# Kernel tuning notes

Hardware: AMD Instinct MI355X
Metric: run time of the kernel (lower is better)

Reference implementation:

```python
import jax, jax.numpy as jnp
import numpy as np

B, S, D, H, W, FFN = 2, 4096, 1024, 16, 256, 4096
HD = D // H


def layer_norm(x, g, b):
    mu = x.mean(-1, keepdims=True)
    var = ((x - mu) ** 2).mean(-1, keepdims=True)
    return (x - mu) * jax.lax.rsqrt(var + 1e-5) * g + b


def setup_inputs() -> dict:
    key = jax.random.key(0)
    ks = jax.random.split(key, 16)
    s = 1.0 / np.sqrt(D)
    inp = {
        "x": jax.random.normal(ks[0], (B, S, D), jnp.float32),
        "Wq": jax.random.normal(ks[1], (D, D), jnp.float32) * s,
        "bq": jnp.zeros((D,), jnp.float32),
        "Wk": jax.random.normal(ks[2], (D, D), jnp.float32) * s,
        "bk": jnp.zeros((D,), jnp.float32),
        "Wv": jax.random.normal(ks[3], (D, D), jnp.float32) * s,
        "bv": jnp.zeros((D,), jnp.float32),
        "Wo": jax.random.normal(ks[4], (D, D), jnp.float32) * s,
        "bo": jnp.zeros((D,), jnp.float32),
        "g1": jnp.ones((D,), jnp.float32),
        "b1": jnp.zeros((D,), jnp.float32),
        "W1": jax.random.normal(ks[5], (D, FFN), jnp.float32) * s,
        "c1": jnp.zeros((FFN,), jnp.float32),
        "W2": jax.random.normal(ks[6], (FFN, D), jnp.float32) * (1.0 / np.sqrt(FFN)),
        "c2": jnp.zeros((D,), jnp.float32),
        "g2": jnp.ones((D,), jnp.float32),
        "b2": jnp.zeros((D,), jnp.float32),
    }
    return inp


def sliding_window_attn(x, Wq, bq, Wk, bk, Wv, bv, Wo, bo):
    b, s, d = x.shape
    nb = s // W
    # project and chunk into blocks of size W: (B, nb, W, H, HD)
    q = (x @ Wq + bq).reshape(b, nb, W, H, HD)
    k = (x @ Wk + bk).reshape(b, nb, W, H, HD)
    v = (x @ Wv + bv).reshape(b, nb, W, H, HD)
    pad = [(0, 0), (1, 1), (0, 0), (0, 0), (0, 0)]
    kp, vp = jnp.pad(k, pad), jnp.pad(v, pad)
    # each block attends to [prev, self, next] blocks -> (B, nb, 3W, H, HD)
    kc = jnp.concatenate([kp[:, :-2], kp[:, 1:-1], kp[:, 2:]], axis=2)
    vc = jnp.concatenate([vp[:, :-2], vp[:, 1:-1], vp[:, 2:]], axis=2)
    scale = jnp.asarray(1.0 / np.sqrt(HD), x.dtype)
    scores = jnp.einsum("bnqhd,bnkhd->bhnqk", q, kc) * scale
    i = jnp.arange(W)[:, None]
    j = jnp.arange(3 * W)[None, :]
    band = jnp.abs(i + W - j) <= W  # (W, 3W): |q_pos - k_pos| <= W
    kidx = jnp.arange(nb)[:, None] * W - W + jnp.arange(3 * W)[None, :]
    valid = (kidx >= 0) & (kidx < s)  # (nb, 3W): drop padded halo blocks
    mask = band[None, :, :] & valid[:, None, :]  # (nb, W, 3W)
    scores = jnp.where(mask[None, None], scores, jnp.asarray(-1e9, x.dtype))
    attn = jax.nn.softmax(scores, axis=-1)
    out = jnp.einsum("bhnqk,bnkhd->bnqhd", attn, vc).reshape(b, s, d)
    return out @ Wo + bo


def reference(x, Wq, bq, Wk, bk, Wv, bv, Wo, bo, g1, b1, W1, c1, W2, c2, g2, b2):
    a = sliding_window_attn(x, Wq, bq, Wk, bk, Wv, bv, Wo, bo)
    h = layer_norm(a + x, g1, b1)  # dropout = identity (eval mode)
    f = jax.nn.gelu(h @ W1 + c1) @ W2 + c2
    return layer_norm(f + h, g2, b2)
```

## Files before the change

kernel.cpp:

```cpp
#include <hip/hip_runtime.h>
#include <hip/hip_bf16.h>

#define BB 2
#define SS 4096
#define DD 1024
#define HH 16
#define WW 256
#define FF 4096
#define HDIM 64
#define NBLK (SS / WW)
#define MROWS (BB * SS)

typedef short bfrag8 __attribute__((ext_vector_type(8)));
typedef float floatx4 __attribute__((ext_vector_type(4)));

__device__ __forceinline__ float bf2f(ushort u) {
    union { uint i; float f; } c; c.i = ((uint)u) << 16; return c.f;
}
__device__ __forceinline__ ushort f2bf(float f) {
    union { float f; uint i; } c; c.f = f;
    uint r = (c.i + 0x7FFFu + ((c.i >> 16) & 1u)) >> 16;
    return (ushort)r;
}
__device__ __forceinline__ float gelu_fast(float x) {
    float z2 = 1.5957691216057308f * x * (1.f + 0.044715f * x * x);
    return x / (1.f + __expf(-z2));
}

__device__ __forceinline__ void gload_lds16(const ushort* g, ushort* l) {
    __builtin_amdgcn_global_load_lds(
        (const __attribute__((address_space(1))) void*)g,
        (__attribute__((address_space(3))) void*)l, 16, 0, 0);
}

__global__ __launch_bounds__(256) void cvt_f32_bf16(
    const float* __restrict__ in, ushort* __restrict__ out)
{
    size_t i = ((size_t)blockIdx.x * 256 + threadIdx.x) * 4;
    float4 v = *(const float4*)(in + i);
    union { ushort u[4]; uint2 d; } t;
    t.u[0] = f2bf(v.x); t.u[1] = f2bf(v.y);
    t.u[2] = f2bf(v.z); t.u[3] = f2bf(v.w);
    *(uint2*)(out + i) = t.d;
}

__global__ __launch_bounds__(256) void cvt_transpose_all(
    const float* __restrict__ Wq, const float* __restrict__ Wk,
    const float* __restrict__ Wv, const float* __restrict__ Wo,
    const float* __restrict__ W1, const float* __restrict__ W2,
    ushort* __restrict__ WqkvT, ushort* __restrict__ WoT,
    ushort* __restrict__ W1t, ushort* __restrict__ W2t)
{
    __shared__ ushort sT[32][33];
    const int z = blockIdx.z;
    const float* in; ushort* out; int K, N, n0, k0;
    if (z < 4) {
        if (blockIdx.x >= 32) return;
        in  = (z == 0) ? Wq : (z == 1) ? Wk : (z == 2) ? Wv : Wo;
        out = (z < 3) ? WqkvT + (size_t)z * 1024 * 1024 : WoT;
        K = 1024; N = 1024;
        n0 = blockIdx.x * 32; k0 = blockIdx.y * 32;
    } else if (z == 4) {
        in = W1; out = W1t; K = 1024; N = 4096;
        n0 = blockIdx.x * 32; k0 = blockIdx.y * 32;
    } else {
        in = W2; out = W2t; K = 4096; N = 1024;
        n0 = blockIdx.y * 32; k0 = blockIdx.x * 32;
    }

    const int r  = threadIdx.x >> 3;
    const int c4 = (threadIdx.x & 7) * 4;

    float4 v = *(const float4*)(in + (size_t)(k0 + r) * N + n0 + c4);
    sT[c4 + 0][r] = f2bf(v.x);
    sT[c4 + 1][r] = f2bf(v.y);
    sT[c4 + 2][r] = f2bf(v.z);
    sT[c4 + 3][r] = f2bf(v.w);
    __syncthreads();
    union { ushort u[4]; uint2 d; } t;
#pragma unroll
    for (int e = 0; e < 4; ++e) t.u[e] = sT[r][c4 + e];
    *(uint2*)(out + (size_t)(n0 + r) * K + k0 + c4) = t.d;
}

__global__ __launch_bounds__(256) void gemm_bt(
    const ushort* __restrict__ A, const ushort* __restrict__ Bt,
    const float* __restrict__ bias, ushort* __restrict__ C,
    int M, int N, int K, int act)
{
    __shared__ ushort sA[128 * 32];
    __shared__ ushort sB[128 * 32];

    const int tid  = threadIdx.x;
    const int m0   = blockIdx.y * 128;
    const int n0   = blockIdx.x * 128;
    const int wave = tid >> 6;
    const int lane = tid & 63;
    const int wm   = (wave >> 1) * 64;
    const int wn   = (wave & 1) * 64;
    const int lrow = lane & 15;
    const int quad = lane >> 4;

    floatx4 acc[4][4];
#pragma unroll
    for (int i = 0; i < 4; ++i)
#pragma unroll
        for (int j = 0; j < 4; ++j)
            acc[i][j] = (floatx4){0.f, 0.f, 0.f, 0.f};

    for (int k0 = 0; k0 < K; k0 += 32) {
#pragma unroll
        for (int it = 0; it < 2; ++it) {
            int c = it * 256 + tid;
            gload_lds16(A  + (size_t)(m0 + (c >> 2)) * K + k0 + (c & 3) * 8, &sA[c * 8]);
            gload_lds16(Bt + (size_t)(n0 + (c >> 2)) * K + k0 + (c & 3) * 8, &sB[c * 8]);
        }
        __syncthreads();

        bfrag8 af[4], bfv[4];
#pragma unroll
        for (int mt = 0; mt < 4; ++mt)
            af[mt] = *(const bfrag8*)&sA[(wm + mt * 16 + lrow) * 32 + quad * 8];
#pragma unroll
        for (int nt = 0; nt < 4; ++nt)
            bfv[nt] = *(const bfrag8*)&sB[(wn + nt * 16 + lrow) * 32 + quad * 8];
#pragma unroll
        for (int mt = 0; mt < 4; ++mt)
#pragma unroll
            for (int nt = 0; nt < 4; ++nt)
                acc[mt][nt] = __builtin_amdgcn_mfma_f32_16x16x32_bf16(
                    bfv[nt], af[mt], acc[mt][nt], 0, 0, 0);
        __syncthreads();
    }

#pragma unroll
    for (int nt = 0; nt < 4; ++nt) {
        int nb = n0 + wn + nt * 16 + quad * 4;
        union { float4 v; float f[4]; } b4;
        b4.v = *(const float4*)(bias + nb);
#pragma unroll
        for (int mt = 0; mt < 4; ++mt) {
            int row = m0 + wm + mt * 16 + lrow;
            union { ushort u[4]; uint2 d; } t;
#pragma unroll
            for (int r = 0; r < 4; ++r) {
                float v = acc[mt][nt][r] + b4.f[r];
                if (act) v = gelu_fast(v);
                t.u[r] = f2bf(v);
            }
            *(uint2*)(C + (size_t)row * N + nb) = t.d;
        }
    }
}

__global__ __launch_bounds__(256) void gemm_qkv(
    const ushort* __restrict__ A, const ushort* __restrict__ Bt,
    const float* __restrict__ bq, const float* __restrict__ bk,
    const float* __restrict__ bv,
    ushort* __restrict__ qb, ushort* __restrict__ kb, ushort* __restrict__ vT)
{
    __shared__ ushort sA[128 * 32];
    __shared__ ushort sB[128 * 32];
    const int K = DD;

    const int tid  = threadIdx.x;
    const int m0   = blockIdx.y * 128;
    const int n0   = blockIdx.x * 128;
    const int wave = tid >> 6;
    const int lane = tid & 63;
    const int wm   = (wave >> 1) * 64;
    const int wn   = (wave & 1) * 64;
    const int lrow = lane & 15;
    const int quad = lane >> 4;
    const int sel  = n0 >> 10;

    floatx4 acc[4][4];
#pragma unroll
    for (int i = 0; i < 4; ++i)
#pragma unroll
        for (int j = 0; j < 4; ++j)
            acc[i][j] = (floatx4){0.f, 0.f, 0.f, 0.f};

    if (sel < 2) {
        for (int k0 = 0; k0 < K; k0 += 32) {
#pragma unroll
            for (int it = 0; it < 2; ++it) {
                int c = it * 256 + tid;
                gload_lds16(A  + (size_t)(m0 + (c >> 2)) * K + k0 + (c & 3) * 8, &sA[c * 8]);
                gload_lds16(Bt + (size_t)(n0 + (c >> 2)) * K + k0 + (c & 3) * 8, &sB[c * 8]);
            }
            __syncthreads();
            bfrag8 af[4], bfv[4];
#pragma unroll
            for (int mt = 0; mt < 4; ++mt)
                af[mt] = *(const bfrag8*)&sA[(wm + mt * 16 + lrow) * 32 + quad * 8];
#pragma unroll
            for (int nt = 0; nt < 4; ++nt)
                bfv[nt] = *(const bfrag8*)&sB[(wn + nt * 16 + lrow) * 32 + quad * 8];
#pragma unroll
            for (int mt = 0; mt < 4; ++mt)
#pragma unroll
                for (int nt = 0; nt < 4; ++nt)
                    acc[mt][nt] = __builtin_amdgcn_mfma_f32_16x16x32_bf16(
                        bfv[nt], af[mt], acc[mt][nt], 0, 0, 0);
            __syncthreads();
        }
        ushort* C = (sel == 0) ? qb : kb;
        const float* bias = (sel == 0) ? bq : bk;
        const int colbase = n0 + wn;
#pragma unroll
        for (int nt = 0; nt < 4; ++nt) {
            int nb = (colbase + nt * 16 + quad * 4) & 1023;
            union { float4 v; float f[4]; } b4;
            b4.v = *(const float4*)(bias + nb);
#pragma unroll
            for (int mt = 0; mt < 4; ++mt) {
                int row = m0 + wm + mt * 16 + lrow;
                union { ushort u[4]; uint2 d; } t;
#pragma unroll
                for (int r = 0; r < 4; ++r) t.u[r] = f2bf(acc[mt][nt][r] + b4.f[r]);
                *(uint2*)(C + (size_t)row * DD + nb) = t.d;
            }
        }
    } else {
        for (int k0 = 0; k0 < K; k0 += 32) {
#pragma unroll
            for (int it = 0; it < 2; ++it) {
                int c = it * 256 + tid;
                gload_lds16(A  + (size_t)(m0 + (c >> 2)) * K + k0 + (c & 3) * 8, &sA[c * 8]);
                gload_lds16(Bt + (size_t)(n0 + (c >> 2)) * K + k0 + (c & 3) * 8, &sB[c * 8]);
            }
            __syncthreads();
            bfrag8 af[4], bfv[4];
#pragma unroll
            for (int mt = 0; mt < 4; ++mt)
                af[mt] = *(const bfrag8*)&sA[(wm + mt * 16 + lrow) * 32 + quad * 8];
#pragma unroll
            for (int nt = 0; nt < 4; ++nt)
                bfv[nt] = *(const bfrag8*)&sB[(wn + nt * 16 + lrow) * 32 + quad * 8];
#pragma unroll
            for (int mt = 0; mt < 4; ++mt)
#pragma unroll
                for (int nt = 0; nt < 4; ++nt)
                    acc[mt][nt] = __builtin_amdgcn_mfma_f32_16x16x32_bf16(
                        af[mt], bfv[nt], acc[mt][nt], 0, 0, 0);
            __syncthreads();
        }
        const int colbase = n0 + wn;
#pragma unroll
        for (int nt = 0; nt < 4; ++nt) {
            int cc = (colbase + nt * 16 + lrow) & 1023;
            int h = cc >> 6, dh = cc & 63;
            float bb = bv[cc];
#pragma unroll
            for (int mt = 0; mt < 4; ++mt) {
                int row0 = m0 + wm + mt * 16 + (quad << 2);
                int b = row0 >> 12, s = row0 & 4095;
                union { ushort u[4]; uint2 d; } t;
#pragma unroll
                for (int r = 0; r < 4; ++r) t.u[r] = f2bf(acc[mt][nt][r] + bb);
                *(uint2*)(vT + (size_t)(((b * HH + h) * HDIM + dh)) * SS + s) = t.d;
            }
        }
    }
}

__global__ __launch_bounds__(64, 2) void attn_flash(
    const ushort* __restrict__ q, const ushort* __restrict__ k,
    const ushort* __restrict__ vT, ushort* __restrict__ out)
{
    __shared__ ushort sP[64 * 72];

    const int qt = blockIdx.x, h = blockIdx.y, b = blockIdx.z;
    const int lane = threadIdx.x;
    const int c16  = lane & 15;
    const int quad = lane >> 4;
    const float CC = 0.18033688011112042f;

    bfrag8 qf[4][2];
    {
        const size_t qbase = ((size_t)b * SS + qt * 64) * DD + h * HDIM;
#pragma unroll
        for (int nt = 0; nt < 4; ++nt)
#pragma unroll
            for (int ks = 0; ks < 2; ++ks)
                qf[nt][ks] = *(const bfrag8*)(q + qbase +
                    (size_t)(nt * 16 + c16) * DD + ks * 32 + quad * 8);
    }

    floatx4 oacc[4][4];
#pragma unroll
    for (int i = 0; i < 4; ++i)
#pragma unroll
        for (int j = 0; j < 4; ++j)
            oacc[i][j] = (floatx4){0.f, 0.f, 0.f, 0.f};
    float mrow[4], lsum[4];
#pragma unroll
    for (int i = 0; i < 4; ++i) { mrow[i] = -1e30f; lsum[i] = 0.f; }

    const int st0 = (qt - 4 > 0) ? qt - 4 : 0;
    const int st1 = (qt + 4 < 63) ? qt + 4 : 63;
    const size_t kb_b  = (size_t)b * SS * DD + h * HDIM;
    const size_t vT_b  = (size_t)((b * HH + h) * HDIM) * SS;

    for (int st = st0; st <= st1; ++st) {
        const int dlt = st - qt;

        floatx4 sacc[4][4];
#pragma unroll
        for (int i = 0; i < 4; ++i)
#pragma unroll
            for (int j = 0; j < 4; ++j)
                sacc[i][j] = (floatx4){0.f, 0.f, 0.f, 0.f};
#pragma unroll
        for (int ks = 0; ks < 2; ++ks) {
            bfrag8 kf[4];
#pragma unroll
            for (int mt = 0; mt < 4; ++mt)
                kf[mt] = *(const bfrag8*)(k + kb_b +
                    (size_t)(st * 64 + mt * 16 + c16) * DD + ks * 32 + quad * 8);
#pragma unroll
            for (int mt = 0; mt < 4; ++mt)
#pragma unroll
                for (int nt = 0; nt < 4; ++nt)
                    sacc[mt][nt] = __builtin_amdgcn_mfma_f32_16x16x32_bf16(
                        kf[mt], qf[nt][ks], sacc[mt][nt], 0, 0, 0);
        }

        if (dlt == 4 || dlt == -4) {
#pragma unroll
            for (int mt = 0; mt < 4; ++mt)
#pragma unroll
                for (int nt = 0; nt < 4; ++nt)
#pragma unroll
                    for (int r = 0; r < 4; ++r) {
                        int kl = mt * 16 + quad * 4 + r;
                        int ql = nt * 16 + c16;
                        bool ok = (dlt < 0) ? (kl >= ql) : (kl <= ql);
                        if (!ok) sacc[mt][nt][r] = -1e30f;
                    }
        }

        float pm[4];
#pragma unroll
        for (int nt = 0; nt < 4; ++nt) {
            float a0 = fmaxf(fmaxf(sacc[0][nt][0], sacc[0][nt][1]),
                             fmaxf(sacc[0][nt][2], sacc[0][nt][3]));
            float a1 = fmaxf(fmaxf(sacc[1][nt][0], sacc[1][nt][1]),
                             fmaxf(sacc[1][nt][2], sacc[1][nt][3]));
            float a2 = fmaxf(fmaxf(sacc[2][nt][0], sacc[2][nt][1]),
                             fmaxf(sacc[2][nt][2], sacc[2][nt][3]));
            float a3 = fmaxf(fmaxf(sacc[3][nt][0], sacc[3][nt][1]),
                             fmaxf(sacc[3][nt][2], sacc[3][nt][3]));
            pm[nt] = fmaxf(fmaxf(a0, a1), fmaxf(a2, a3));
            pm[nt] = fmaxf(pm[nt], __shfl_xor(pm[nt], 16, 64));
            pm[nt] = fmaxf(pm[nt], __shfl_xor(pm[nt], 32, 64));
        }
        float al[4];
#pragma unroll
        for (int nt = 0; nt < 4; ++nt) {
            float mn = fmaxf(mrow[nt], pm[nt]);
            al[nt] = exp2f((mrow[nt] - mn) * CC);
            mrow[nt] = mn;
        }
        float ps[4] = {0.f, 0.f, 0.f, 0.f};
#pragma unroll
        for (int mt = 0; mt < 4; ++mt)
#pragma unroll
            for (int nt = 0; nt < 4; ++nt)
#pragma unroll
                for (int r = 0; r < 4; ++r) {
                    float p = exp2f((sacc[mt][nt][r] - mrow[nt]) * CC);
                    sacc[mt][nt][r] = p;
                    ps[nt] += p;
                }
#pragma unroll
        for (int nt = 0; nt < 4; ++nt) {
            ps[nt] += __shfl_xor(ps[nt], 16, 64);
            ps[nt] += __shfl_xor(ps[nt], 32, 64);
            lsum[nt] = lsum[nt] * al[nt] + ps[nt];
        }

#pragma unroll
        for (int mt = 0; mt < 4; ++mt)
#pragma unroll
            for (int nt = 0; nt < 4; ++nt) {
                int row = nt * 16 + c16;
                int g   = (2 * mt + (quad >> 1)) ^ (row & 3);
                union { ushort u[4]; uint2 d; } t;
#pragma unroll
                for (int r = 0; r < 4; ++r) t.u[r] = f2bf(sacc[mt][nt][r]);
                *(uint2*)&sP[row * 72 + g * 8 + (quad & 1) * 4] = t.d;
            }

#pragma unroll
        for (int dt = 0; dt < 4; ++dt)
#pragma unroll
            for (int nq = 0; nq < 4; ++nq)
#pragma unroll
                for (int r = 0; r < 4; ++r)
                    oacc[dt][nq][r] *= al[nq];

#pragma unroll
        for (int ks = 0; ks < 2; ++ks) {
            bfrag8 vf[4], pf[4];
#pragma unroll
            for (int dt = 0; dt < 4; ++dt)
                vf[dt] = *(const bfrag8*)(vT + vT_b +
                    (size_t)(dt * 16 + c16) * SS + st * 64 + ks * 32 + quad * 8);
#pragma unroll
            for (int nq = 0; nq < 4; ++nq) {
                int row = nq * 16 + c16;
                int g   = (4 * ks + quad) ^ (row & 3);
                pf[nq] = *(const bfrag8*)&sP[row * 72 + g * 8];
            }
#pragma unroll
            for (int dt = 0; dt < 4; ++dt)
#pragma unroll
                for (int nq = 0; nq < 4; ++nq)
                    oacc[dt][nq] = __builtin_amdgcn_mfma_f32_16x16x32_bf16(
                        vf[dt], pf[nq], oacc[dt][nq], 0, 0, 0);
        }
    }

#pragma unroll
    for (int nq = 0; nq < 4; ++nq) {
        float inv = 1.f / lsum[nq];
        size_t rbase = ((size_t)b * SS + qt * 64 + nq * 16 + c16) * DD + h * HDIM;
#pragma unroll
        for (int dt = 0; dt < 4; ++dt) {
            union { ushort u[4]; uint2 d; } t;
#pragma unroll
            for (int r = 0; r < 4; ++r) t.u[r] = f2bf(oacc[dt][nq][r] * inv);
            *(uint2*)(out + rbase + dt * 16 + quad * 4) = t.d;
        }
    }
}

__device__ __forceinline__ float ldv(const float* p)  { return *p; }
__device__ __forceinline__ float ldv(const ushort* p) { return bf2f(*p); }
__device__ __forceinline__ void  stv(float* p, float v)  { *p = v; }
__device__ __forceinline__ void  stv(ushort* p, float v) { *p = f2bf(v); }

template <typename RT, typename OT>
__global__ __launch_bounds__(256) void add_ln(
    const ushort* __restrict__ a, const RT* __restrict__ res,
    const float* __restrict__ g, const float* __restrict__ bb,
    OT* __restrict__ out)
{
    const int row = blockIdx.x;
    const int tid = threadIdx.x;
    const size_t base = (size_t)row * DD + tid * 4;

    float x[4];
    float s1 = 0.f, s2 = 0.f;
#pragma unroll
    for (int e = 0; e < 4; ++e) {
        x[e] = bf2f(a[base + e]) + ldv(res + base + e);
        s1 += x[e];
        s2 += x[e] * x[e];
    }
#pragma unroll
    for (int off = 32; off > 0; off >>= 1) {
        s1 += __shfl_down(s1, off, 64);
        s2 += __shfl_down(s2, off, 64);
    }
    __shared__ float r1[4], r2[4];
    const int wave = tid >> 6, lane = tid & 63;
    if (lane == 0) { r1[wave] = s1; r2[wave] = s2; }
    __syncthreads();
    float t1 = r1[0] + r1[1] + r1[2] + r1[3];
    float t2 = r2[0] + r2[1] + r2[2] + r2[3];
    float mu  = t1 * (1.f / DD);
    float var = t2 * (1.f / DD) - mu * mu;
    float rs  = rsqrtf(var + 1e-5f);

#pragma unroll
    for (int e = 0; e < 4; ++e) {
        int col = tid * 4 + e;
        float y = (x[e] - mu) * rs * g[col] + bb[col];
        stv(out + base + e, y);
    }
}

extern "C" void kernel_launch(void* const* d_in, const int* in_sizes, int n_in,
                              void* d_out, int out_size, void* d_ws, size_t ws_size,
                              hipStream_t stream)
{
    (void)in_sizes; (void)n_in; (void)out_size; (void)ws_size;

    const float* x  = (const float*)d_in[0];
    const float* Wq = (const float*)d_in[1];
    const float* bq = (const float*)d_in[2];
    const float* Wk = (const float*)d_in[3];
    const float* bk = (const float*)d_in[4];
    const float* Wv = (const float*)d_in[5];
    const float* bv = (const float*)d_in[6];
    const float* Wo = (const float*)d_in[7];
    const float* bo = (const float*)d_in[8];
    const float* g1 = (const float*)d_in[9];
    const float* b1 = (const float*)d_in[10];
    const float* W1 = (const float*)d_in[11];
    const float* c1 = (const float*)d_in[12];
    const float* W2 = (const float*)d_in[13];
    const float* c2 = (const float*)d_in[14];
    const float* g2 = (const float*)d_in[15];
    const float* b2 = (const float*)d_in[16];
    float* outp = (float*)d_out;

    char* ws = (char*)d_ws;
    const size_t MB = 1024 * 1024;
    ushort* WqkvT = (ushort*)(ws);
    ushort* WoT = (ushort*)(ws + 6  * MB);
    ushort* W1t = (ushort*)(ws + 8  * MB);
    ushort* W2t = (ushort*)(ws + 16 * MB);
    ushort* xb  = (ushort*)(ws + 24 * MB);
    ushort* qb  = (ushort*)(ws + 40 * MB);
    ushort* kb  = (ushort*)(ws + 56 * MB);
    ushort* vT  = (ushort*)(ws + 72 * MB);
    ushort* att = (ushort*)(ws + 88 * MB);
    ushort* aproj = qb;
    ushort* hbuf  = att;
    ushort* m1  = (ushort*)(ws + 24 * MB);
    ushort* fbuf = (ushort*)(ws + 104 * MB);

    dim3 blk(256, 1, 1);
    dim3 gD(DD / 128, MROWS / 128, 1);
    dim3 gQKV(3 * DD / 128, MROWS / 128, 1);
    dim3 gF(FF / 128, MROWS / 128, 1);
    dim3 ga(SS / 64, HH, BB);
    dim3 gl(MROWS, 1, 1);

    hipLaunchKernelGGL(cvt_transpose_all, dim3(128, 32, 6), blk, 0, stream,
                       Wq, Wk, Wv, Wo, W1, W2, WqkvT, WoT, W1t, W2t);
    hipLaunchKernelGGL(cvt_f32_bf16, dim3(8192), blk, 0, stream, x, xb);

    hipLaunchKernelGGL(gemm_qkv, gQKV, blk, 0, stream, xb, WqkvT, bq, bk, bv, qb, kb, vT);

    hipLaunchKernelGGL(attn_flash, ga, dim3(64, 1, 1), 0, stream, qb, kb, vT, att);

    hipLaunchKernelGGL(gemm_bt, gD, blk, 0, stream, att, WoT, bo, aproj, MROWS, DD, DD, 0);
    hipLaunchKernelGGL((add_ln<float, ushort>), gl, blk, 0, stream, aproj, x, g1, b1, hbuf);

    hipLaunchKernelGGL(gemm_bt, gF, blk, 0, stream, hbuf, W1t, c1, m1, MROWS, FF, DD, 1);
    hipLaunchKernelGGL(gemm_bt, gD, blk, 0, stream, m1, W2t, c2, fbuf, MROWS, DD, FF, 0);
    hipLaunchKernelGGL((add_ln<ushort, float>), gl, blk, 0, stream, fbuf, hbuf, g2, b2, outp);
}
```

Before: 573.8 us.

## Deepen GEMM K-tile to 64 with XOR-swizzled LDS and grouped block ordering

Both GEMM kernels now stage 64-wide K slices instead of 32, which halves the number of barrier pairs per output tile. LDS columns are XOR-swizzled by row to avoid bank conflicts on fragment reads. A 1D grid is remapped so that consecutive blocks are spread across 8 groups of M-tiles, aiming for better L2/MALL locality across XCDs. The QKV kernel also merges its duplicated K-loops into one loop with a branch on the MFMA operand order. LDS use doubles per block, which may lower occupancy.

```diff
diff --git a/kernel.cpp b/kernel.cpp
--- a/kernel.cpp
+++ b/kernel.cpp
@@ -88,12 +88,16 @@
     const float* __restrict__ bias, ushort* __restrict__ C,
     int M, int N, int K, int act)
 {
-    __shared__ ushort sA[128 * 32];
-    __shared__ ushort sB[128 * 32];
+    __shared__ ushort sA[128 * 64];
+    __shared__ ushort sB[128 * 64];
 
     const int tid  = threadIdx.x;
-    const int m0   = blockIdx.y * 128;
-    const int n0   = blockIdx.x * 128;
+    const int nx   = N >> 7;
+    const int nyg  = (M >> 7) >> 3;
+    const int gid  = blockIdx.x;
+    const int j    = gid >> 3;
+    const int m0   = ((gid & 7) * nyg + j / nx) * 128;
+    const int n0   = (j % nx) * 128;
     const int wave = tid >> 6;
     const int lane = tid & 63;
     const int wm   = (wave >> 1) * 64;
@@ -105,31 +109,42 @@
 #pragma unroll
     for (int i = 0; i < 4; ++i)
 #pragma unroll
-        for (int j = 0; j < 4; ++j)
-            acc[i][j] = (floatx4){0.f, 0.f, 0.f, 0.f};
-
-    for (int k0 = 0; k0 < K; k0 += 32) {
-#pragma unroll
-        for (int it = 0; it < 2; ++it) {
-            int c = it * 256 + tid;
-            gload_lds16(A  + (size_t)(m0 + (c >> 2)) * K + k0 + (c & 3) * 8, &sA[c * 8]);
-            gload_lds16(Bt + (size_t)(n0 + (c >> 2)) * K + k0 + (c & 3) * 8, &sB[c * 8]);
+        for (int j2 = 0; j2 < 4; ++j2)
+            acc[i][j2] = (floatx4){0.f, 0.f, 0.f, 0.f};
+
+    for (int k0 = 0; k0 < K; k0 += 64) {
+#pragma unroll
+        for (int it = 0; it < 4; ++it) {
+            int c    = it * 256 + tid;
+            int row  = c >> 3;
+            int scol = ((c ^ (row & 7)) & 7) << 3;
+            gload_lds16(A  + (size_t)(m0 + row) * K + k0 + scol, &sA[c * 8]);
+            gload_lds16(Bt + (size_t)(n0 + row) * K + k0 + scol, &sB[c * 8]);
         }
         __syncthreads();
 
-        bfrag8 af[4], bfv[4];
-#pragma unroll
-        for (int mt = 0; mt < 4; ++mt)
-            af[mt] = *(const bfrag8*)&sA[(wm + mt * 16 + lrow) * 32 + quad * 8];
-#pragma unroll
-        for (int nt = 0; nt < 4; ++nt)
-            bfv[nt] = *(const bfrag8*)&sB[(wn + nt * 16 + lrow) * 32 + quad * 8];
-#pragma unroll
-        for (int mt = 0; mt < 4; ++mt)
-#pragma unroll
-            for (int nt = 0; nt < 4; ++nt)
-                acc[mt][nt] = __builtin_amdgcn_mfma_f32_16x16x32_bf16(
-                    bfv[nt], af[mt], acc[mt][nt], 0, 0, 0);
+#pragma unroll
+        for (int ks = 0; ks < 2; ++ks) {
+            bfrag8 af[4], bfv[4];
+#pragma unroll
+            for (int mt = 0; mt < 4; ++mt) {
+                int row = wm + mt * 16 + lrow;
+                int G   = ks * 4 + quad;
+                af[mt] = *(const bfrag8*)&sA[row * 64 + (((G ^ row) & 7) << 3) + ((G >> 3) << 6)];
+            }
+#pragma unroll
+            for (int nt = 0; nt < 4; ++nt) {
+                int row = wn + nt * 16 + lrow;
+                int G   = ks * 4 + quad;
+                bfv[nt] = *(const bfrag8*)&sB[row * 64 + (((G ^ row) & 7) << 3) + ((G >> 3) << 6)];
+            }
+#pragma unroll
+            for (int mt = 0; mt < 4; ++mt)
+#pragma unroll
+                for (int nt = 0; nt < 4; ++nt)
+                    acc[mt][nt] = __builtin_amdgcn_mfma_f32_16x16x32_bf16(
+                        bfv[nt], af[mt], acc[mt][nt], 0, 0, 0);
+        }
         __syncthreads();
     }
 
@@ -159,13 +174,16 @@
     const float* __restrict__ bv,
     ushort* __restrict__ qb, ushort* __restrict__ kb, ushort* __restrict__ vT)
 {
-    __shared__ ushort sA[128 * 32];
-    __shared__ ushort sB[128 * 32];
+    __shared__ ushort sA[128 * 64];
+    __shared__ ushort sB[128 * 64];
     const int K = DD;
 
     const int tid  = threadIdx.x;
-    const int m0   = blockIdx.y * 128;
-    const int n0   = blockIdx.x * 128;
+    const int nx   = 24, nyg = 8;
+    const int gid  = blockIdx.x;
+    const int j    = gid >> 3;
+    const int m0   = ((gid & 7) * nyg + j / nx) * 128;
+    const int n0   = (j % nx) * 128;
     const int wave = tid >> 6;
     const int lane = tid & 63;
     const int wm   = (wave >> 1) * 64;
@@ -178,33 +196,55 @@
 #pragma unroll
     for (int i = 0; i < 4; ++i)
 #pragma unroll
-        for (int j = 0; j < 4; ++j)
-            acc[i][j] = (floatx4){0.f, 0.f, 0.f, 0.f};
+        for (int j2 = 0; j2 < 4; ++j2)
+            acc[i][j2] = (floatx4){0.f, 0.f, 0.f, 0.f};
+
+    for (int k0 = 0; k0 < K; k0 += 64) {
+#pragma unroll
+        for (int it = 0; it < 4; ++it) {
+            int c    = it * 256 + tid;
+            int row  = c >> 3;
+            int scol = ((c ^ (row & 7)) & 7) << 3;
+            gload_lds16(A  + (size_t)(m0 + row) * K + k0 + scol, &sA[c * 8]);
+            gload_lds16(Bt + (size_t)(n0 + row) * K + k0 + scol, &sB[c * 8]);
+        }
+        __syncthreads();
+
+#pragma unroll
+        for (int ks = 0; ks < 2; ++ks) {
+            bfrag8 af[4], bfv[4];
+#pragma unroll
+            for (int mt = 0; mt < 4; ++mt) {
+                int row = wm + mt * 16 + lrow;
+                int G   = ks * 4 + quad;
+                af[mt] = *(const bfrag8*)&sA[row * 64 + (((G ^ row) & 7) << 3)];
+            }
+#pragma unroll
+            for (int nt = 0; nt < 4; ++nt) {
+                int row = wn + nt * 16 + lrow;
+                int G   = ks * 4 + quad;
+                bfv[nt] = *(const bfrag8*)&sB[row * 64 + (((G ^ row) & 7) << 3)];
+            }
+            if (sel < 2) {
+#pragma unroll
+                for (int mt = 0; mt < 4; ++mt)
+#pragma unroll
+                    for (int nt = 0; nt < 4; ++nt)
+                        acc[mt][nt] = __builtin_amdgcn_mfma_f32_16x16x32_bf16(
+                            bfv[nt], af[mt], acc[mt][nt], 0, 0, 0);
+            } else {
+#pragma unroll
+                for (int mt = 0; mt < 4; ++mt)
+#pragma unroll
+                    for (int nt = 0; nt < 4; ++nt)
+                        acc[mt][nt] = __builtin_amdgcn_mfma_f32_16x16x32_bf16(
+                            af[mt], bfv[nt], acc[mt][nt], 0, 0, 0);
+            }
+        }
+        __syncthreads();
+    }
 
     if (sel < 2) {
-        for (int k0 = 0; k0 < K; k0 += 32) {
-#pragma unroll
-            for (int it = 0; it < 2; ++it) {
-                int c = it * 256 + tid;
-                gload_lds16(A  + (size_t)(m0 + (c >> 2)) * K + k0 + (c & 3) * 8, &sA[c * 8]);
-                gload_lds16(Bt + (size_t)(n0 + (c >> 2)) * K + k0 + (c & 3) * 8, &sB[c * 8]);
-            }
-            __syncthreads();
-            bfrag8 af[4], bfv[4];
-#pragma unroll
-            for (int mt = 0; mt < 4; ++mt)
-                af[mt] = *(const bfrag8*)&sA[(wm + mt * 16 + lrow) * 32 + quad * 8];
-#pragma unroll
-            for (int nt = 0; nt < 4; ++nt)
-                bfv[nt] = *(const bfrag8*)&sB[(wn + nt * 16 + lrow) * 32 + quad * 8];
-#pragma unroll
-            for (int mt = 0; mt < 4; ++mt)
-#pragma unroll
-                for (int nt = 0; nt < 4; ++nt)
-                    acc[mt][nt] = __builtin_amdgcn_mfma_f32_16x16x32_bf16(
-                        bfv[nt], af[mt], acc[mt][nt], 0, 0, 0);
-            __syncthreads();
-        }
         ushort* C = (sel == 0) ? qb : kb;
         const float* bias = (sel == 0) ? bq : bk;
         const int colbase = n0 + wn;
@@ -223,29 +263,6 @@
             }
         }
     } else {
-        for (int k0 = 0; k0 < K; k0 += 32) {
-#pragma unroll
-            for (int it = 0; it < 2; ++it) {
-                int c = it * 256 + tid;
-                gload_lds16(A  + (size_t)(m0 + (c >> 2)) * K + k0 + (c & 3) * 8, &sA[c * 8]);
-                gload_lds16(Bt + (size_t)(n0 + (c >> 2)) * K + k0 + (c & 3) * 8, &sB[c * 8]);
-            }
-            __syncthreads();
-            bfrag8 af[4], bfv[4];
-#pragma unroll
-            for (int mt = 0; mt < 4; ++mt)
-                af[mt] = *(const bfrag8*)&sA[(wm + mt * 16 + lrow) * 32 + quad * 8];
-#pragma unroll
-            for (int nt = 0; nt < 4; ++nt)
-                bfv[nt] = *(const bfrag8*)&sB[(wn + nt * 16 + lrow) * 32 + quad * 8];
-#pragma unroll
-            for (int mt = 0; mt < 4; ++mt)
-#pragma unroll
-                for (int nt = 0; nt < 4; ++nt)
-                    acc[mt][nt] = __builtin_amdgcn_mfma_f32_16x16x32_bf16(
-                        af[mt], bfv[nt], acc[mt][nt], 0, 0, 0);
-            __syncthreads();
-        }
         const int colbase = n0 + wn;
 #pragma unroll
         for (int nt = 0; nt < 4; ++nt) {
@@ -525,9 +542,9 @@
     ushort* fbuf = (ushort*)(ws + 104 * MB);
 
     dim3 blk(256, 1, 1);
-    dim3 gD(DD / 128, MROWS / 128, 1);
-    dim3 gQKV(3 * DD / 128, MROWS / 128, 1);
-    dim3 gF(FF / 128, MROWS / 128, 1);
+    dim3 gD1((DD / 128) * (MROWS / 128), 1, 1);
+    dim3 gQKV1((3 * DD / 128) * (MROWS / 128), 1, 1);
+    dim3 gF1((FF / 128) * (MROWS / 128), 1, 1);
     dim3 ga(SS / 64, HH, BB);
     dim3 gl(MROWS, 1, 1);
 
@@ -535,14 +552,14 @@
                        Wq, Wk, Wv, Wo, W1, W2, WqkvT, WoT, W1t, W2t);
     hipLaunchKernelGGL(cvt_f32_bf16, dim3(8192), blk, 0, stream, x, xb);
 
-    hipLaunchKernelGGL(gemm_qkv, gQKV, blk, 0, stream, xb, WqkvT, bq, bk, bv, qb, kb, vT);
+    hipLaunchKernelGGL(gemm_qkv, gQKV1, blk, 0, stream, xb, WqkvT, bq, bk, bv, qb, kb, vT);
 
     hipLaunchKernelGGL(attn_flash, ga, dim3(64, 1, 1), 0, stream, qb, kb, vT, att);
 
-    hipLaunchKernelGGL(gemm_bt, gD, blk, 0, stream, att, WoT, bo, aproj, MROWS, DD, DD, 0);
+    hipLaunchKernelGGL(gemm_bt, gD1, blk, 0, stream, att, WoT, bo, aproj, MROWS, DD, DD, 0);
     hipLaunchKernelGGL((add_ln<float, ushort>), gl, blk, 0, stream, aproj, x, g1, b1, hbuf);
 
-    hipLaunchKernelGGL(gemm_bt, gF, blk, 0, stream, hbuf, W1t, c1, m1, MROWS, FF, DD, 1);
-    hipLaunchKernelGGL(gemm_bt, gD, blk, 0, stream, m1, W2t, c2, fbuf, MROWS, DD, FF, 0);
+    hipLaunchKernelGGL(gemm_bt, gF1, blk, 0, stream, hbuf, W1t, c1, m1, MROWS, FF, DD, 1);
+    hipLaunchKernelGGL(gemm_bt, gD1, blk, 0, stream, m1, W2t, c2, fbuf, MROWS, DD, FF, 0);
     hipLaunchKernelGGL((add_ln<ushort, float>), gl, blk, 0, stream, fbuf, hbuf, g2, b2, outp);
 }
```

Measured after the change: 491.7 us. 14.3% less time.
